# Optimization experiments

Hardware: AMD Instinct MI355X
Metric: run time of the kernel (lower is better)

The kernel has to match this reference:

```python
import jax, jax.numpy as jnp
import numpy as np


def setup_inputs() -> dict:
    key = jax.random.key(0)
    k1, k2, k3 = jax.random.split(key, 3)
    dim, heads, dim_head, rows = 512, 8, 64, 64
    b, t = 4, 256
    _dim = heads * dim_head
    x = jax.random.normal(k1, (b * rows, t, dim), dtype=jnp.float32)
    # torch nn.Linear weight layout: [out_features, in_features]
    W_qkv = jax.random.normal(k2, (3 * _dim, dim), dtype=jnp.float32) * (dim ** -0.5)
    W0 = jax.random.normal(k3, (dim, _dim), dtype=jnp.float32) * (_dim ** -0.5)
    return {"x": x, "W_qkv": W_qkv, "W0": W0, "rows": rows, "heads": heads}


def reference(x, W_qkv, W0, rows, heads):
    br, t, dim = x.shape
    b = br // rows
    three_dim = W_qkv.shape[0]
    dim_head = three_dim // (3 * heads)
    scale = (rows * dim_head) ** -0.5

    qkv = x @ W_qkv.T  # [(b*rows), t, 3*heads*dim_head]
    # einops '(b rows) t (d k h) -> k b rows h t d': last dim ordered (d, k, h)
    qkv = qkv.reshape(b, rows, t, dim_head, 3, heads)
    qkv = jnp.transpose(qkv, (4, 0, 1, 5, 2, 3))  # [3, b, rows, h, t, d]
    q, k, v = qkv[0], qkv[1], qkv[2]

    # tied-row attention: sum QK^T over rows before a single shared softmax
    scores = jnp.einsum('brhid,brhjd->bhij', q, k) * scale  # [b, h, t, t]
    attn = jax.nn.softmax(scores, axis=-1)
    # broadcast shared attention map back across rows
    out = jnp.einsum('bhij,brhjd->brhid', attn, v)  # [b, rows, h, t, d]
    # 'b rows h t d -> (b rows) t (h d)'
    out = jnp.transpose(out, (0, 1, 3, 2, 4)).reshape(br, t, heads * dim_head)
    return out @ W0.T
```

## Files before the change

kernel.cpp:

```cpp
#include <hip/hip_runtime.h>


typedef short  bf16x8 __attribute__((ext_vector_type(8)));
typedef float  f32x4  __attribute__((ext_vector_type(4)));

#define MFMA16(a,b,c) __builtin_amdgcn_mfma_f32_16x16x32_bf16((a),(b),(c),0,0,0)

__device__ __forceinline__ ushort f2bf(float f) {
  union { float f; unsigned u; } v; v.f = f;
  unsigned r = v.u + 0x7fffu + ((v.u >> 16) & 1u);
  return (ushort)(r >> 16);
}

__device__ __forceinline__ void gload_lds16(const void* g, void* lds) {
  __builtin_amdgcn_global_load_lds(
      (const __attribute__((address_space(1))) void*)g,
      (__attribute__((address_space(3))) void*)lds, 16, 0, 0);
}


__global__ void cast_f32_to_bf16(const float* __restrict__ in,
                                 ushort* __restrict__ out, int n4) {
  int idx = blockIdx.x * blockDim.x + threadIdx.x;
  int stride = gridDim.x * blockDim.x;
  for (int v = idx; v < n4; v += stride) {
    float4 f = reinterpret_cast<const float4*>(in)[v];
    ushort4 o; o.x = f2bf(f.x); o.y = f2bf(f.y); o.z = f2bf(f.z); o.w = f2bf(f.w);
    reinterpret_cast<ushort4*>(out)[v] = o;
  }
}

__global__ void permute_wqkv_k(const float* __restrict__ W, ushort* __restrict__ Wp) {
  int np = blockIdx.x;
  int k = np >> 9, h = (np >> 6) & 7, d = np & 63;
  const float4* s = reinterpret_cast<const float4*>(W + (size_t)(d * 24 + k * 8 + h) * 512);
  ushort4* o = reinterpret_cast<ushort4*>(Wp + (size_t)np * 512);
  for (int c = threadIdx.x; c < 128; c += blockDim.x) {
    float4 f = s[c];
    ushort4 u; u.x = f2bf(f.x); u.y = f2bf(f.y); u.z = f2bf(f.z); u.w = f2bf(f.w);
    o[c] = u;
  }
}


__device__ __forceinline__ void gemm_nt_256x128(
    const ushort* __restrict__ A, const ushort* __restrict__ B,
    int lda, int ldb, int P, int m0, int n0, char* lds, f32x4 (&acc)[8][4]) {
  const int tid = threadIdx.x;
  const int w = tid >> 6, l = tid & 63;
  const int il = l & 15, kl = l >> 4;
  const int wm = w >> 1, wn = w & 1;

  auto stageA = [&](char* buf, int kt) {
#pragma unroll
    for (int c = 0; c < 4; ++c) {
      int rbase = (w << 6) + (c << 4);
      int row = rbase + (l >> 2);
      int s = ((l & 3) - ((row >> 1) & 3)) & 3;
      gload_lds16(A + (size_t)(m0 + row) * lda + (kt << 5) + (s << 3),
                  buf + rbase * 64);
    }
  };
  auto stageB = [&](char* buf, int kt) {
#pragma unroll
    for (int c = 0; c < 2; ++c) {
      int rbase = (w << 5) + (c << 4);
      int row = rbase + (l >> 2);
      int s = ((l & 3) - ((row >> 1) & 3)) & 3;
      gload_lds16(B + (size_t)(n0 + row) * ldb + (kt << 5) + (s << 3),
                  buf + 16384 + rbase * 64);
    }
  };
  auto loadA8 = [&](const char* buf, bf16x8 (&af)[8]) {
#pragma unroll
    for (int q = 0; q < 8; ++q) {
      int row = (wm << 7) + (q << 4) + il;
      af[q] = *(const bf16x8*)(buf + row * 64 + (((kl + (row >> 1)) & 3) << 4));
    }
  };
  auto loadB4 = [&](const char* buf, bf16x8 (&bfr)[4]) {
#pragma unroll
    for (int q = 0; q < 4; ++q) {
      int row = (wn << 6) + (q << 4) + il;
      bfr[q] = *(const bf16x8*)(buf + 16384 + row * 64 + (((kl + (row >> 1)) & 3) << 4));
    }
  };

#pragma unroll
  for (int i = 0; i < 8; ++i)
#pragma unroll
    for (int j = 0; j < 4; ++j) acc[i][j] = f32x4{0.f, 0.f, 0.f, 0.f};

  stageA(lds, 0);         stageB(lds, 0);
  stageA(lds + 24576, 1); stageB(lds + 24576, 1);
  asm volatile("s_waitcnt vmcnt(6)" ::: "memory");
  __builtin_amdgcn_s_barrier();

  int cur = 0, nx = 2;
  for (int g = 0; g < P; ++g) {
    char* cbuf = lds + cur * 24576;
    char* sbuf = lds + nx * 24576;
    bf16x8 af[8], bfr[4];
    loadA8(cbuf, af);
    loadB4(cbuf, bfr);
    if (g + 2 < P) { stageA(sbuf, g + 2); stageB(sbuf, g + 2); }
    __builtin_amdgcn_s_setprio(1);
#pragma unroll
    for (int fm = 0; fm < 8; ++fm)
#pragma unroll
      for (int fn = 0; fn < 4; ++fn)
        acc[fm][fn] = MFMA16(af[fm], bfr[fn], acc[fm][fn]);
    __builtin_amdgcn_s_setprio(0);
    if (g + 2 < P) asm volatile("s_waitcnt vmcnt(6)" ::: "memory");
    else           asm volatile("s_waitcnt vmcnt(0)" ::: "memory");
    __builtin_amdgcn_s_barrier();
    cur = (cur == 2) ? 0 : cur + 1;
    nx  = (nx  == 2) ? 0 : nx  + 1;
  }
}


__global__ __launch_bounds__(256, 2) void gemm_qkv_k(
    const ushort* __restrict__ xb, const ushort* __restrict__ Wp,
    ushort* __restrict__ Qb, ushort* __restrict__ Kb, ushort* __restrict__ Vt) {
  __shared__ __align__(16) char lds[73728];
  f32x4 acc[8][4];
  const int Bid = blockIdx.x;
  const int xcd = Bid & 7, idx = Bid >> 3;
  const int nt = idx % 12, pl = idx / 12;
  const int m0 = ((pl << 3) + xcd) << 8;
  const int n0 = nt << 7;
  gemm_nt_256x128(xb, Wp, 512, 512, 16, m0, n0, lds, acc);

  const int tid = threadIdx.x, w = tid >> 6, l = tid & 63;
  const int il = l & 15, kl = l >> 4;
  const int wm = w >> 1, wn = w & 1;
  const int kq = n0 >> 9;
  const int br = m0 >> 8, b = br >> 6, r = br & 63;

  if (kq < 2) {
    ushort* dstb = kq ? Kb : Qb;
#pragma unroll
    for (int fm = 0; fm < 8; ++fm)
#pragma unroll
      for (int fn = 0; fn < 4; ++fn) {
        int n = n0 + (wn << 6) + (fn << 4) + il;
        int h = (n >> 6) & 7, d = n & 63;
#pragma unroll
        for (int j = 0; j < 4; ++j) {
          int i = (wm << 7) + (fm << 4) + (kl << 2) + j;
          size_t dst = ((size_t)((((b << 3) + h) << 8) + i) << 12) + (r << 6) + d;
          dstb[dst] = f2bf(acc[fm][fn][j]);
        }
      }
  } else {
#pragma unroll
    for (int fm = 0; fm < 8; ++fm)
#pragma unroll
      for (int fn = 0; fn < 4; ++fn) {
        int n = n0 - 1024 + (wn << 6) + (fn << 4) + il;
        int h = n >> 6, d = n & 63;
        int i0 = (wm << 7) + (fm << 4) + (kl << 2);
        size_t dst = (((size_t)((((b << 3) + h) << 12)) + (r << 6) + d) << 8) + i0;
        ushort4 pk; pk.x = f2bf(acc[fm][fn][0]); pk.y = f2bf(acc[fm][fn][1]);
        pk.z = f2bf(acc[fm][fn][2]); pk.w = f2bf(acc[fm][fn][3]);
        *reinterpret_cast<ushort4*>(&Vt[dst]) = pk;
      }
  }
}


__global__ __launch_bounds__(256, 2) void gemm_out_k(
    const ushort* __restrict__ O2, const ushort* __restrict__ W0b,
    float* __restrict__ out) {
  __shared__ __align__(16) char lds[73728];
  f32x4 acc[8][4];
  const int Bid = blockIdx.x;
  const int xcd = Bid & 7, idx = Bid >> 3;
  const int nt = idx & 3, pl = idx >> 2;
  const int m0 = ((pl << 3) + xcd) << 8;
  const int n0 = nt << 7;
  gemm_nt_256x128(O2, W0b, 512, 512, 16, m0, n0, lds, acc);

  const int tid = threadIdx.x, w = tid >> 6, l = tid & 63;
  const int il = l & 15, kl = l >> 4;
  const int wm = w >> 1, wn = w & 1;
#pragma unroll
  for (int fm = 0; fm < 8; ++fm)
#pragma unroll
    for (int fn = 0; fn < 4; ++fn) {
      int n = n0 + (wn << 6) + (fn << 4) + il;
#pragma unroll
      for (int j = 0; j < 4; ++j) {
        int m = m0 + (wm << 7) + (fm << 4) + (kl << 2) + j;
        out[(size_t)m * 512 + n] = acc[fm][fn][j];
      }
    }
}


__global__ __launch_bounds__(256, 2) void gemm_s_k(
    const ushort* __restrict__ Qb, const ushort* __restrict__ Kb,
    float* __restrict__ Sp) {
  __shared__ __align__(16) char lds[73728];
  f32x4 acc[8][4];
  const int Bid = blockIdx.x;
  const int xcd = Bid & 7, idx = Bid >> 3;
  const int nt = idx & 1, zl = idx >> 1;
  const int z = (zl << 3) + xcd;
  const int bh = z >> 3, ks = z & 7;
  const int n0 = nt << 7;
  const size_t base = ((size_t)bh << 20) + ((size_t)ks << 9);
  gemm_nt_256x128(Qb + base, Kb + base, 4096, 4096, 16, 0, n0, lds, acc);

  const int tid = threadIdx.x, w = tid >> 6, l = tid & 63;
  const int il = l & 15, kl = l >> 4;
  const int wm = w >> 1, wn = w & 1;
  float* o = Sp + ((size_t)z << 16);
#pragma unroll
  for (int fm = 0; fm < 8; ++fm)
#pragma unroll
    for (int fn = 0; fn < 4; ++fn) {
      int n = n0 + (wn << 6) + (fn << 4) + il;
#pragma unroll
      for (int j = 0; j < 4; ++j) {
        int m = (wm << 7) + (fm << 4) + (kl << 2) + j;
        o[(size_t)m * 256 + n] = acc[fm][fn][j];
      }
    }
}


__global__ void softmax_k(const float* __restrict__ Sp, ushort* __restrict__ Pb) {
  const int w = threadIdx.x >> 6, l = threadIdx.x & 63;
  const int row = (blockIdx.x << 2) + w;
  const int bh = row >> 8, i = row & 255;
  const float4* p0 = reinterpret_cast<const float4*>(
      Sp + (((size_t)bh << 3) << 16) + ((size_t)i << 8)) + l;
  float s0 = 0.f, s1 = 0.f, s2 = 0.f, s3 = 0.f;
#pragma unroll
  for (int ks = 0; ks < 8; ++ks) {
    float4 a = p0[(size_t)ks * 16384];
    s0 += a.x; s1 += a.y; s2 += a.z; s3 += a.w;
  }
  const float scale = 0.015625f;
  s0 *= scale; s1 *= scale; s2 *= scale; s3 *= scale;
  float m = fmaxf(fmaxf(s0, s1), fmaxf(s2, s3));
#pragma unroll
  for (int d2 = 1; d2 < 64; d2 <<= 1) m = fmaxf(m, __shfl_xor(m, d2));
  float e0 = __expf(s0 - m), e1 = __expf(s1 - m);
  float e2 = __expf(s2 - m), e3 = __expf(s3 - m);
  float sum = e0 + e1 + e2 + e3;
#pragma unroll
  for (int d2 = 1; d2 < 64; d2 <<= 1) sum += __shfl_xor(sum, d2);
  float r = 1.0f / sum;
  ushort4 p; p.x = f2bf(e0 * r); p.y = f2bf(e1 * r);
  p.z = f2bf(e2 * r); p.w = f2bf(e3 * r);
  reinterpret_cast<ushort4*>(Pb + ((size_t)bh << 16) + ((size_t)i << 8))[l] = p;
}


__global__ __launch_bounds__(256, 2) void gemm_pv_k(
    const ushort* __restrict__ Vt, const ushort* __restrict__ Pb,
    ushort* __restrict__ O2) {
  __shared__ __align__(16) char lds[73728];
  f32x4 acc[8][4];
  const int Bid = blockIdx.x;
  const int xcd = Bid & 7, idx = Bid >> 3;
  const int sub = idx & 31, grp = idx >> 5;
  const int bh = (grp << 3) + xcd, b = bh >> 3, h = bh & 7;
  const int m0 = (sub >> 1) << 8;
  const int n0 = (sub & 1) << 7;
  gemm_nt_256x128(Vt + ((size_t)bh << 20), Pb + ((size_t)bh << 16),
                  256, 256, 8, m0, n0, lds, acc);

  const int tid = threadIdx.x, w = tid >> 6, l = tid & 63;
  const int il = l & 15, kl = l >> 4;
  const int wm = w >> 1, wn = w & 1;
#pragma unroll
  for (int fm = 0; fm < 8; ++fm) {
    int rd0 = m0 + (wm << 7) + (fm << 4) + (kl << 2);
    int r = rd0 >> 6, d0 = rd0 & 63;
#pragma unroll
    for (int fn = 0; fn < 4; ++fn) {
      int i = n0 + (wn << 6) + (fn << 4) + il;
      ushort4 pk; pk.x = f2bf(acc[fm][fn][0]); pk.y = f2bf(acc[fm][fn][1]);
      pk.z = f2bf(acc[fm][fn][2]); pk.w = f2bf(acc[fm][fn][3]);
      *reinterpret_cast<ushort4*>(
          O2 + ((size_t)((((b << 6) + r) << 8) + i) << 9) + (h << 6) + d0) = pk;
    }
  }
}


extern "C" void kernel_launch(void* const* d_in, const int* in_sizes, int n_in,
                              void* d_out, int out_size, void* d_ws, size_t ws_size,
                              hipStream_t stream) {
  const float* x    = (const float*)d_in[0];
  const float* Wqkv = (const float*)d_in[1];
  const float* W0   = (const float*)d_in[2];
  float* out = (float*)d_out;

  char* ws = (char*)d_ws;
  ushort* xb  = (ushort*)(ws);
  ushort* Wp  = (ushort*)(ws + 67108864);
  ushort* W0b = (ushort*)(ws + 68681728);
  ushort* Qb  = (ushort*)(ws + 69206016);
  ushort* Kb  = (ushort*)(ws + 136314880);
  ushort* Vt  = (ushort*)(ws + 203423744);
  if (ws_size < 270532608ull) return;

  cast_f32_to_bf16<<<2048, 256, 0, stream>>>(x, xb, 8388608);
  cast_f32_to_bf16<<<256, 256, 0, stream>>>(W0, W0b, 65536);
  permute_wqkv_k<<<1536, 128, 0, stream>>>(Wqkv, Wp);

  gemm_qkv_k<<<3072, 256, 0, stream>>>(xb, Wp, Qb, Kb, Vt);

  float*  Sp = (float*)xb;
  ushort* Pb = Qb;
  ushort* O2 = xb;

  gemm_s_k<<<512, 256, 0, stream>>>(Qb, Kb, Sp);
  softmax_k<<<2048, 256, 0, stream>>>(Sp, Pb);
  gemm_pv_k<<<1024, 256, 0, stream>>>(Vt, Pb, O2);

  gemm_out_k<<<1024, 256, 0, stream>>>(O2, W0b, out);
}
```

Before: 303.5 us.

## Stage Q/K epilogue through LDS, halve score split-K, merge weight prep kernels

The Q/K epilogue of the QKV GEMM now writes bf16 results into LDS first, then issues 16-byte vectorized global stores instead of scattered 2-byte stores. The score GEMM drops from 8-way to 4-way split-K (256 blocks, longer K loop), which halves the fp32 partial-score traffic the softmax must read. The two weight prep kernels are merged into one launch. The trade-off is fewer score-GEMM blocks (only 256, about one per CU) and extra LDS syncs in the QKV epilogue.

```diff
diff --git a/kernel.cpp b/kernel.cpp
--- a/kernel.cpp
+++ b/kernel.cpp
@@ -30,15 +30,26 @@
   }
 }
 
-__global__ void permute_wqkv_k(const float* __restrict__ W, ushort* __restrict__ Wp) {
-  int np = blockIdx.x;
-  int k = np >> 9, h = (np >> 6) & 7, d = np & 63;
-  const float4* s = reinterpret_cast<const float4*>(W + (size_t)(d * 24 + k * 8 + h) * 512);
-  ushort4* o = reinterpret_cast<ushort4*>(Wp + (size_t)np * 512);
-  for (int c = threadIdx.x; c < 128; c += blockDim.x) {
-    float4 f = s[c];
+__global__ void prep_k(const float* __restrict__ W, ushort* __restrict__ Wp,
+                       const float* __restrict__ W0, ushort* __restrict__ W0b) {
+  const int bid = blockIdx.x, tid = threadIdx.x;
+  if (bid < 768) {
+    int np = (bid << 1) + (tid >> 7);
+    int c  = tid & 127;
+    int k = np >> 9, h = (np >> 6) & 7, d = np & 63;
+    float4 f = reinterpret_cast<const float4*>(
+        W + (size_t)(d * 24 + k * 8 + h) * 512)[c];
     ushort4 u; u.x = f2bf(f.x); u.y = f2bf(f.y); u.z = f2bf(f.z); u.w = f2bf(f.w);
-    o[c] = u;
+    reinterpret_cast<ushort4*>(Wp + (size_t)np * 512)[c] = u;
+  } else {
+    int v0 = ((bid - 768) << 10) + (tid << 2);
+#pragma unroll
+    for (int q = 0; q < 4; ++q) {
+      int v = v0 + q;
+      float4 f = reinterpret_cast<const float4*>(W0)[v];
+      ushort4 u; u.x = f2bf(f.x); u.y = f2bf(f.y); u.z = f2bf(f.z); u.w = f2bf(f.w);
+      reinterpret_cast<ushort4*>(W0b)[v] = u;
+    }
   }
 }
 
@@ -139,20 +150,31 @@
   const int br = m0 >> 8, b = br >> 6, r = br & 63;
 
   if (kq < 2) {
-    ushort* dstb = kq ? Kb : Qb;
+    ushort* Pl = (ushort*)lds;
+    __syncthreads();
 #pragma unroll
     for (int fm = 0; fm < 8; ++fm)
 #pragma unroll
       for (int fn = 0; fn < 4; ++fn) {
-        int n = n0 + (wn << 6) + (fn << 4) + il;
-        int h = (n >> 6) & 7, d = n & 63;
+        int ccol = (wn << 6) + (fn << 4) + il;
 #pragma unroll
         for (int j = 0; j < 4; ++j) {
-          int i = (wm << 7) + (fm << 4) + (kl << 2) + j;
-          size_t dst = ((size_t)((((b << 3) + h) << 8) + i) << 12) + (r << 6) + d;
-          dstb[dst] = f2bf(acc[fm][fn][j]);
+          int irow = (wm << 7) + (fm << 4) + (kl << 2) + j;
+          Pl[irow * 136 + ccol] = f2bf(acc[fm][fn][j]);
         }
       }
+    __syncthreads();
+    ushort* dstb = kq ? Kb : Qb;
+#pragma unroll
+    for (int it = 0; it < 16; ++it) {
+      int u = (it << 8) + tid;
+      int row = u >> 4, n8 = (u & 15);
+      int n_full = n0 + (n8 << 3);
+      int h = (n_full >> 6) & 7, d0 = n_full & 63;
+      bf16x8 v = *(const bf16x8*)(Pl + row * 136 + (n8 << 3));
+      size_t dst = ((size_t)((((b << 3) + h) << 8) + row) << 12) + (r << 6) + d0;
+      *reinterpret_cast<bf16x8*>(&dstb[dst]) = v;
+    }
   } else {
 #pragma unroll
     for (int fm = 0; fm < 8; ++fm)
@@ -205,13 +227,11 @@
   __shared__ __align__(16) char lds[73728];
   f32x4 acc[8][4];
   const int Bid = blockIdx.x;
-  const int xcd = Bid & 7, idx = Bid >> 3;
-  const int nt = idx & 1, zl = idx >> 1;
-  const int z = (zl << 3) + xcd;
-  const int bh = z >> 3, ks = z & 7;
+  const int nt = Bid & 1, z = Bid >> 1;
+  const int bh = z >> 2, ks = z & 3;
   const int n0 = nt << 7;
-  const size_t base = ((size_t)bh << 20) + ((size_t)ks << 9);
-  gemm_nt_256x128(Qb + base, Kb + base, 4096, 4096, 16, 0, n0, lds, acc);
+  const size_t base = ((size_t)bh << 20) + ((size_t)ks << 10);
+  gemm_nt_256x128(Qb + base, Kb + base, 4096, 4096, 32, 0, n0, lds, acc);
 
   const int tid = threadIdx.x, w = tid >> 6, l = tid & 63;
   const int il = l & 15, kl = l >> 4;
@@ -236,15 +256,13 @@
   const int row = (blockIdx.x << 2) + w;
   const int bh = row >> 8, i = row & 255;
   const float4* p0 = reinterpret_cast<const float4*>(
-      Sp + (((size_t)bh << 3) << 16) + ((size_t)i << 8)) + l;
-  float s0 = 0.f, s1 = 0.f, s2 = 0.f, s3 = 0.f;
-#pragma unroll
-  for (int ks = 0; ks < 8; ++ks) {
-    float4 a = p0[(size_t)ks * 16384];
-    s0 += a.x; s1 += a.y; s2 += a.z; s3 += a.w;
-  }
+      Sp + (((size_t)bh << 2) << 16) + ((size_t)i << 8)) + l;
+  float4 a = p0[0], b2 = p0[16384], c = p0[32768], d = p0[49152];
   const float scale = 0.015625f;
-  s0 *= scale; s1 *= scale; s2 *= scale; s3 *= scale;
+  float s0 = (a.x + b2.x + c.x + d.x) * scale;
+  float s1 = (a.y + b2.y + c.y + d.y) * scale;
+  float s2 = (a.z + b2.z + c.z + d.z) * scale;
+  float s3 = (a.w + b2.w + c.w + d.w) * scale;
   float m = fmaxf(fmaxf(s0, s1), fmaxf(s2, s3));
 #pragma unroll
   for (int d2 = 1; d2 < 64; d2 <<= 1) m = fmaxf(m, __shfl_xor(m, d2));
@@ -311,8 +329,7 @@
   if (ws_size < 270532608ull) return;
 
   cast_f32_to_bf16<<<2048, 256, 0, stream>>>(x, xb, 8388608);
-  cast_f32_to_bf16<<<256, 256, 0, stream>>>(W0, W0b, 65536);
-  permute_wqkv_k<<<1536, 128, 0, stream>>>(Wqkv, Wp);
+  prep_k<<<832, 256, 0, stream>>>(Wqkv, Wp, W0, W0b);
 
   gemm_qkv_k<<<3072, 256, 0, stream>>>(xb, Wp, Qb, Kb, Vt);
 
@@ -320,7 +337,7 @@
   ushort* Pb = Qb;
   ushort* O2 = xb;
 
-  gemm_s_k<<<512, 256, 0, stream>>>(Qb, Kb, Sp);
+  gemm_s_k<<<256, 256, 0, stream>>>(Qb, Kb, Sp);
   softmax_k<<<2048, 256, 0, stream>>>(Sp, Pb);
   gemm_pv_k<<<1024, 256, 0, stream>>>(Vt, Pb, O2);
 
```

New measurement: 309.8 us. 2.1% more time.
